# Kernel tuning notes

Hardware: AMD Instinct MI355X
Metric: run time of the kernel (lower is better)

The kernel has to match this reference:

```python
import jax, jax.numpy as jnp
import numpy as np

A, B, N, D, E = 2, 128, 50000, 512, 4096  # atomics, batch, entities, feat dim, nnz per sparse row-matrix
CLIP = 1e-14


def setup_inputs() -> dict:
    key = jax.random.key(0)
    ks = jax.random.split(key, 7)
    return {
        "entity_embedding": jax.random.normal(ks[0], (N, D), jnp.float32) * 0.02,
        "head_vector": jax.random.uniform(ks[1], (A, B, N), jnp.float32),
        "head_emb": jax.random.normal(ks[2], (A, B, D), jnp.float32),
        "pred_emb": jax.random.normal(ks[3], (A, B, D), jnp.float32),
        "edge_val": jax.random.uniform(ks[4], (A, B, E), jnp.float32),
        "edge_src": jax.random.randint(ks[5], (A, B, E), 0, N),
        "edge_dst": jax.random.randint(ks[6], (A, B, E), 0, N),
    }


def clip_norm(v):
    # masked_fill(v < clip, 0) / max(clip, sum(v, -1))
    v = jnp.where(v < CLIP, 0.0, v)
    return v / jnp.maximum(CLIP, jnp.sum(v, axis=-1, keepdims=True))


def reference(entity_embedding, head_vector, head_emb, pred_emb, edge_val, edge_src, edge_dst):
    a, b, n = head_vector.shape
    # --- symbolic message passing: per-(atomic, batch) sparse spmv via gather/scatter ---
    # msg over edge e: val[e] * head_vector[src[e]], scattered into dst[e]
    msgs = edge_val * jnp.take_along_axis(head_vector, edge_src, axis=-1)  # [A,B,E]
    offs = (jnp.arange(a * b, dtype=edge_dst.dtype) * n).reshape(a, b, 1)
    flat_idx = (edge_dst + offs).reshape(-1)
    symbolic = (
        jnp.zeros((a * b * n,), head_vector.dtype)
        .at[flat_idx].add(msgs.reshape(-1))
        .reshape(a, b, n)
    )
    symbolic = clip_norm(symbolic)
    # --- neural enhancement: estimate tail emb (TransE-style), softmax KGE scores over all entities ---
    tail_emb = head_emb + pred_emb                                  # estimate_tail_emb
    score = jnp.einsum('abd,nd->abn', tail_emb, entity_embedding)   # kge_similarity
    neural = jax.nn.softmax(score, axis=-1)                         # [A,B,N]
    enhanced = clip_norm(symbolic + neural)
    # --- product conjunction over atomics targeting the same free term ---
    agg = clip_norm(jnp.prod(enhanced, axis=0))                     # [B,N]
    # --- fuzzy_vector_to_embedding ---
    out_emb = agg @ entity_embedding                                # [B,D]
    return out_emb
```

## Files before the change

kernel.cpp:

```cpp
#include <hip/hip_runtime.h>
#include <hip/hip_bf16.h>
#include <cstdint>
#include <cstddef>

#define A_ 2
#define B_ 128
#define N_ 50000
#define D_ 512
#define E_ 4096
#define AB_ 256
#define CLIPV 1e-14f

static const size_t OFF_SYM   = 0;
static const size_t OFF_SCORE = 12800000;
static const size_t OFF_AGG   = 19200000;
static const size_t OFF_TAIL  = 25600000;
static const size_t OFF_STATS = 25731072;
#define ST_SYMSUM 0
#define ST_EXPSUM 512
#define ST_AGGSUM 1024
#define CH_K 768
#define OCHUNK 66
#define PSTRIDE 800
#define SBLKS 782

typedef __attribute__((ext_vector_type(8))) short short8;
typedef __attribute__((ext_vector_type(4))) float f32x4;

__device__ __forceinline__ unsigned short to_bf16(float f) {
    __hip_bfloat16 bh = __float2bfloat16(f);
    return *reinterpret_cast<unsigned short*>(&bh);
}
__device__ __forceinline__ float bf16f(unsigned short b) {
    return __uint_as_float(((unsigned int)b) << 16);
}
__device__ __forceinline__ void gld_lds16(const unsigned short* g, unsigned short* l) {
    __builtin_amdgcn_global_load_lds(
        (const __attribute__((address_space(1))) void*)g,
        (__attribute__((address_space(3))) void*)l, 16, 0, 0);
}
__device__ __forceinline__ short8 cvt8(const float4& a, const float4& b) {
    short8 h;
    h[0]=(short)to_bf16(a.x); h[1]=(short)to_bf16(a.y); h[2]=(short)to_bf16(a.z); h[3]=(short)to_bf16(a.w);
    h[4]=(short)to_bf16(b.x); h[5]=(short)to_bf16(b.y); h[6]=(short)to_bf16(b.z); h[7]=(short)to_bf16(b.w);
    return h;
}

__global__ __launch_bounds__(256) void k_tail(const float* __restrict__ head,
                                              const float* __restrict__ pred,
                                              unsigned short* __restrict__ tail_hi) {
    int i = blockIdx.x * 256 + threadIdx.x;
    if (i < AB_ * D_) {
        float t = head[i] + pred[i];
        tail_hi[i] = to_bf16(t);
    }
}

__global__ __launch_bounds__(256) void k_scatter(const float* __restrict__ hv,
                                                 const float* __restrict__ ev,
                                                 const int* __restrict__ es,
                                                 const int* __restrict__ ed,
                                                 float* __restrict__ sym,
                                                 float* __restrict__ stats) {
    int ab = blockIdx.x;
    float* symr = sym + (size_t)ab * N_;
    float4 z = make_float4(0.f, 0.f, 0.f, 0.f);
    float4* symv = reinterpret_cast<float4*>(symr);
    for (int i = threadIdx.x; i < 12500; i += 256) symv[i] = z;
    __syncthreads();
    const float* hvr = hv + (size_t)ab * N_;
    int base = ab * E_;
    float local = 0.f;
    for (int e = threadIdx.x; e < E_; e += 256) {
        float v = ev[base + e];
        int s = es[base + e];
        int d = ed[base + e];
        float m = v * hvr[s];
        local += m;
        atomicAdd(&symr[d], m);
    }
    __shared__ float red[256];
    red[threadIdx.x] = local;
    __syncthreads();
    for (int st = 128; st > 0; st >>= 1) {
        if (threadIdx.x < st) red[threadIdx.x] += red[threadIdx.x + st];
        __syncthreads();
    }
    if (threadIdx.x == 0) stats[ST_SYMSUM + ab] = red[0];
}

#define SCB_OFF 8192
#define SBPITCH 32

__global__ __launch_bounds__(256) void k_score(const float* __restrict__ ent,
                                               const unsigned short* __restrict__ tail_hi,
                                               unsigned short* __restrict__ p_out,
                                               float* __restrict__ parts) {
    __shared__ unsigned short lds[12288];
    const int tid = threadIdx.x;
    const int w = tid >> 6;
    const int l = tid & 63;
    const int lm = l & 15;
    const int kg = l >> 4;
    const int n0 = blockIdx.x * 64;
    const int m0w = w * 64;

    f32x4 acc[4][4];
    #pragma unroll
    for (int i = 0; i < 4; ++i)
        #pragma unroll
        for (int j = 0; j < 4; ++j) acc[i][j] = (f32x4){0.f, 0.f, 0.f, 0.f};

    const int arow_base = w * 16 + (l >> 2);
    const int ak = (l & 3) * 8;
    const int bn = tid >> 2;
    const int bc = tid & 3;
    int entrow = n0 + bn;
    if (entrow > N_ - 1) entrow = N_ - 1;
    const float* entp = ent + (size_t)entrow * D_ + bc * 8;

    float4 rB0 = *reinterpret_cast<const float4*>(entp);
    float4 rB1 = *reinterpret_cast<const float4*>(entp + 4);

    for (int t = 0; t < 16; ++t) {
        const int k0 = t * 32;
        #pragma unroll
        for (int i = 0; i < 4; ++i) {
            int row = arow_base + i * 64;
            gld_lds16(tail_hi + (size_t)row * D_ + k0 + ak, &lds[w * 512 + i * 2048]);
        }
        *reinterpret_cast<short8*>(&lds[SCB_OFF + bn * SBPITCH + bc * 8]) = cvt8(rB0, rB1);
        __syncthreads();
        if (t < 15) {
            const int k1 = k0 + 32;
            rB0 = *reinterpret_cast<const float4*>(entp + k1);
            rB1 = *reinterpret_cast<const float4*>(entp + k1 + 4);
        }
        short8 bh[4];
        #pragma unroll
        for (int nj = 0; nj < 4; ++nj) {
            int br = nj * 16 + lm;
            bh[nj] = *reinterpret_cast<const short8*>(&lds[SCB_OFF + br * SBPITCH + kg * 8]);
        }
        #pragma unroll
        for (int mi = 0; mi < 4; ++mi) {
            int ar = m0w + mi * 16 + lm;
            short8 ah = *reinterpret_cast<const short8*>(&lds[ar * 32 + kg * 8]);
            #pragma unroll
            for (int nj = 0; nj < 4; ++nj)
                acc[mi][nj] = __builtin_amdgcn_mfma_f32_16x16x32_bf16(ah, bh[nj], acc[mi][nj], 0, 0, 0);
        }
        if (t < 15) __syncthreads();
    }

    #pragma unroll
    for (int mi = 0; mi < 4; ++mi) {
        #pragma unroll
        for (int j = 0; j < 4; ++j) {
            int row = m0w + mi * 16 + kg * 4 + j;
            float rsum = 0.f;
            #pragma unroll
            for (int nj = 0; nj < 4; ++nj) {
                int col = n0 + nj * 16 + lm;
                if (col < N_) {
                    float pv = expf(acc[mi][nj][j]);
                    p_out[(size_t)row * N_ + col] = to_bf16(pv);
                    rsum += pv;
                }
            }
            rsum += __shfl_xor(rsum, 1);
            rsum += __shfl_xor(rsum, 2);
            rsum += __shfl_xor(rsum, 4);
            rsum += __shfl_xor(rsum, 8);
            if (lm == 0) parts[(size_t)row * PSTRIDE + blockIdx.x] = rsum;
        }
    }
}

__global__ __launch_bounds__(256) void k_expred(const float* __restrict__ parts,
                                                float* __restrict__ stats) {
    int row = blockIdx.x;
    float s = 0.f;
    for (int c = threadIdx.x; c < SBLKS; c += 256) s += parts[(size_t)row * PSTRIDE + c];
    __shared__ float red[256];
    red[threadIdx.x] = s;
    __syncthreads();
    for (int st = 128; st > 0; st >>= 1) {
        if (threadIdx.x < st) red[threadIdx.x] += red[threadIdx.x + st];
        __syncthreads();
    }
    if (threadIdx.x == 0) stats[ST_EXPSUM + row] = red[0];
}

__global__ __launch_bounds__(256) void k_enhagg(const unsigned short* __restrict__ p,
                                                const float* __restrict__ sym,
                                                float* __restrict__ agg,
                                                float* __restrict__ stats) {
    int b = blockIdx.x >> 2, part = blockIdx.x & 3;
    size_t off0 = (size_t)b * N_ + part * 12500;
    size_t off1 = (size_t)(128 + b) * N_ + part * 12500;
    float is0 = 1.f / fmaxf(CLIPV, stats[ST_SYMSUM + b]);
    float is1 = 1.f / fmaxf(CLIPV, stats[ST_SYMSUM + 128 + b]);
    float ie0 = 1.f / fmaxf(CLIPV, stats[ST_EXPSUM + b]);
    float ie1 = 1.f / fmaxf(CLIPV, stats[ST_EXPSUM + 128 + b]);
    const float4* s0p = reinterpret_cast<const float4*>(sym + off0);
    const float4* s1p = reinterpret_cast<const float4*>(sym + off1);
    const ushort4* p0p = reinterpret_cast<const ushort4*>(p + off0);
    const ushort4* p1p = reinterpret_cast<const ushort4*>(p + off1);
    float4* aggp = reinterpret_cast<float4*>(agg + off0);
    float local = 0.f;
    for (int i = threadIdx.x; i < 3125; i += 256) {
        float4 s0 = s0p[i], s1 = s1p[i];
        ushort4 q0 = p0p[i], q1 = p1p[i];
        float sv0[4] = {s0.x, s0.y, s0.z, s0.w};
        float sv1[4] = {s1.x, s1.y, s1.z, s1.w};
        float qv0[4] = {bf16f(q0.x), bf16f(q0.y), bf16f(q0.z), bf16f(q0.w)};
        float qv1[4] = {bf16f(q1.x), bf16f(q1.y), bf16f(q1.z), bf16f(q1.w)};
        float vv[4];
        #pragma unroll
        for (int c = 0; c < 4; ++c) {
            float a0 = (sv0[c] < CLIPV) ? 0.f : sv0[c];
            float a1 = (sv1[c] < CLIPV) ? 0.f : sv1[c];
            float e0 = a0 * is0 + qv0[c] * ie0; e0 = (e0 < CLIPV) ? 0.f : e0;
            float e1 = a1 * is1 + qv1[c] * ie1; e1 = (e1 < CLIPV) ? 0.f : e1;
            float v = e0 * e1 * 0.25f;
            v = (v < CLIPV) ? 0.f : v;
            local += v;
            vv[c] = v;
        }
        float4 o; o.x = vv[0]; o.y = vv[1]; o.z = vv[2]; o.w = vv[3];
        aggp[i] = o;
    }
    __shared__ float red[256];
    red[threadIdx.x] = local;
    __syncthreads();
    for (int st = 128; st > 0; st >>= 1) {
        if (threadIdx.x < st) red[threadIdx.x] += red[threadIdx.x + st];
        __syncthreads();
    }
    if (threadIdx.x == 0) atomicAdd(&stats[ST_AGGSUM + b], red[0]);
}

#define APITCH 40
#define OG_BUF 10240
#define OLDS_B 5120

__global__ __launch_bounds__(256) void k_outgemm(const float* __restrict__ ent,
                                                 const float* __restrict__ aggf,
                                                 float* __restrict__ part) {
    __shared__ unsigned short lds[20480];
    const int bid = blockIdx.x;
    const int chunk = bid >> 2, dt = bid & 3;
    const int n0 = chunk * CH_K, d0 = dt * 128;
    const int tid = threadIdx.x;
    const int w = tid >> 6;
    const int l = tid & 63;
    const int lm = l & 15;
    const int kg = l >> 4;
    const int m0w = (w >> 1) * 64;
    const int c0w = (w & 1) * 64;

    f32x4 acc[4][4];
    #pragma unroll
    for (int i = 0; i < 4; ++i)
        #pragma unroll
        for (int j = 0; j < 4; ++j) acc[i][j] = (f32x4){0.f, 0.f, 0.f, 0.f};

    const int arow = tid >> 1;
    const int ahalf = tid & 1;
    const int dcol = tid & 127;
    const int bhalf = tid >> 7;
    const size_t entcol = (size_t)(d0 + dcol);

    float ra[16], rb[16];

    auto loadA = [&](int k0) {
        int nbase = n0 + k0 + ahalf * 16;
        const float* asrc = aggf + (size_t)arow * N_ + nbase;
        #pragma unroll
        for (int c = 0; c < 2; ++c) {
            if (nbase + c * 8 + 7 < N_) {
                float4 g0 = *reinterpret_cast<const float4*>(asrc + c * 8);
                float4 g1 = *reinterpret_cast<const float4*>(asrc + c * 8 + 4);
                ra[c*8+0]=g0.x; ra[c*8+1]=g0.y; ra[c*8+2]=g0.z; ra[c*8+3]=g0.w;
                ra[c*8+4]=g1.x; ra[c*8+5]=g1.y; ra[c*8+6]=g1.z; ra[c*8+7]=g1.w;
            } else {
                #pragma unroll
                for (int j = 0; j < 8; ++j) {
                    int n = nbase + c * 8 + j;
                    ra[c*8+j] = (n < N_) ? aggf[(size_t)arow * N_ + n] : 0.f;
                }
            }
        }
    };
    auto loadB = [&](int k0) {
        int nb = n0 + k0 + bhalf * 16;
        #pragma unroll
        for (int j = 0; j < 16; ++j) {
            int n = nb + j;
            if (n > N_ - 1) n = N_ - 1;
            rb[j] = ent[(size_t)n * D_ + entcol];
        }
    };
    auto stage = [&](int bufbase) {
        #pragma unroll
        for (int c = 0; c < 2; ++c) {
            short8 hb;
            #pragma unroll
            for (int j = 0; j < 8; ++j) hb[j] = (short)to_bf16(ra[c*8+j]);
            *reinterpret_cast<short8*>(&lds[bufbase + arow * APITCH + ahalf * 16 + c * 8]) = hb;
        }
        #pragma unroll
        for (int c = 0; c < 2; ++c) {
            short8 hb;
            #pragma unroll
            for (int j = 0; j < 8; ++j) hb[j] = (short)to_bf16(rb[c*8+j]);
            *reinterpret_cast<short8*>(&lds[bufbase + OLDS_B + dcol * APITCH + bhalf * 16 + c * 8]) = hb;
        }
    };

    loadA(0); loadB(0);
    stage(0);
    loadA(32); loadB(32);
    __syncthreads();

    for (int t = 0; t < 24; ++t) {
        const int base = (t & 1) * OG_BUF;
        const int nb2 = ((t + 1) & 1) * OG_BUF;
        if (t < 23) stage(nb2);
        if (t < 22) { loadA((t + 2) * 32); loadB((t + 2) * 32); }
        short8 ah[4], bh[4];
        #pragma unroll
        for (int mi = 0; mi < 4; ++mi) {
            int r = m0w + mi * 16 + lm;
            ah[mi] = *reinterpret_cast<const short8*>(&lds[base + r * APITCH + kg * 8]);
        }
        #pragma unroll
        for (int nj = 0; nj < 4; ++nj) {
            int r = c0w + nj * 16 + lm;
            bh[nj] = *reinterpret_cast<const short8*>(&lds[base + OLDS_B + r * APITCH + kg * 8]);
        }
        #pragma unroll
        for (int mi = 0; mi < 4; ++mi)
            #pragma unroll
            for (int nj = 0; nj < 4; ++nj)
                acc[mi][nj] = __builtin_amdgcn_mfma_f32_16x16x32_bf16(ah[mi], bh[nj], acc[mi][nj], 0, 0, 0);
        __syncthreads();
    }

    float* pbase = part + (size_t)chunk * 65536;
    #pragma unroll
    for (int nj = 0; nj < 4; ++nj) {
        int dcolo = d0 + c0w + nj * 16 + lm;
        #pragma unroll
        for (int mi = 0; mi < 4; ++mi) {
            int brow = m0w + mi * 16 + kg * 4;
            #pragma unroll
            for (int j = 0; j < 4; ++j)
                pbase[(size_t)(brow + j) * 512 + dcolo] = acc[mi][nj][j];
        }
    }
}

__global__ __launch_bounds__(256) void k_redout(const float* __restrict__ part,
                                                const float* __restrict__ stats,
                                                float* __restrict__ out) {
    int i = blockIdx.x * 256 + threadIdx.x;
    int b = i >> 9;
    float s = 0.f;
    for (int c = 0; c < OCHUNK; ++c) s += part[(size_t)c * 65536 + i];
    out[i] = s / fmaxf(CLIPV, stats[ST_AGGSUM + b]);
}

extern "C" void kernel_launch(void* const* d_in, const int* in_sizes, int n_in,
                              void* d_out, int out_size, void* d_ws, size_t ws_size,
                              hipStream_t stream) {
    const float* ent = (const float*)d_in[0];
    const float* hv  = (const float*)d_in[1];
    const float* he  = (const float*)d_in[2];
    const float* pe  = (const float*)d_in[3];
    const float* ev  = (const float*)d_in[4];
    const int*   es  = (const int*)d_in[5];
    const int*   ed  = (const int*)d_in[6];
    float* out = (float*)d_out;
    float* ws = (float*)d_ws;

    unsigned short* tail_hi = (unsigned short*)(ws + OFF_TAIL);
    unsigned short* p_bf16 = (unsigned short*)(ws + OFF_SCORE);
    float* parts = ws + OFF_AGG;
    float* aggf  = ws + OFF_AGG;
    float* stats = ws + OFF_STATS;

    hipMemsetAsync(stats, 0, 2048 * sizeof(float), stream);

    k_tail<<<512, 256, 0, stream>>>(he, pe, tail_hi);
    k_scatter<<<AB_, 256, 0, stream>>>(hv, ev, es, ed, ws + OFF_SYM, stats);
    k_score<<<SBLKS, 256, 0, stream>>>(ent, tail_hi, p_bf16, parts);
    k_expred<<<AB_, 256, 0, stream>>>(parts, stats);
    k_enhagg<<<B_ * 4, 256, 0, stream>>>(p_bf16, ws + OFF_SYM, aggf, stats);
    k_outgemm<<<OCHUNK * 4, 256, 0, stream>>>(ent, aggf, ws + OFF_SYM);
    k_redout<<<256, 256, 0, stream>>>(ws + OFF_SYM, stats, out);
}
```

Before: 194.7 us.

## Double K-step to 64 and XOR-swizzle LDS tiles in score GEMM

The score GEMM kernel now loads a 64-wide K slice per iteration instead of 32, which halves the loop trips and the barriers. A and B tiles in LDS use a 64-element row pitch with an XOR swizzle on 8-element chunks to avoid bank conflicts on the MFMA operand reads. LDS use per block grows from about 24KB to 40KB, and more B registers are prefetched, which may lower occupancy.

```diff
diff --git a/kernel.cpp b/kernel.cpp
--- a/kernel.cpp
+++ b/kernel.cpp
@@ -89,14 +89,13 @@
     if (threadIdx.x == 0) stats[ST_SYMSUM + ab] = red[0];
 }
 
-#define SCB_OFF 8192
-#define SBPITCH 32
+#define SCB_OFF 16384
 
 __global__ __launch_bounds__(256) void k_score(const float* __restrict__ ent,
                                                const unsigned short* __restrict__ tail_hi,
                                                unsigned short* __restrict__ p_out,
                                                float* __restrict__ parts) {
-    __shared__ unsigned short lds[12288];
+    __shared__ unsigned short lds[20480];
     const int tid = threadIdx.x;
     const int w = tid >> 6;
     const int l = tid & 63;
@@ -111,46 +110,58 @@
         #pragma unroll
         for (int j = 0; j < 4; ++j) acc[i][j] = (f32x4){0.f, 0.f, 0.f, 0.f};
 
-    const int arow_base = w * 16 + (l >> 2);
-    const int ak = (l & 3) * 8;
+    const int arow_off = l >> 3;
+    const int asrc_kc = ((l & 7) ^ (l >> 3)) * 8;
     const int bn = tid >> 2;
-    const int bc = tid & 3;
+    const int bs = tid & 3;
     int entrow = n0 + bn;
     if (entrow > N_ - 1) entrow = N_ - 1;
-    const float* entp = ent + (size_t)entrow * D_ + bc * 8;
+    const float* entp = ent + (size_t)entrow * D_ + bs * 16;
+    const int bw0 = ((2 * bs)     ^ (bn & 7)) * 8;
+    const int bw1 = ((2 * bs + 1) ^ (bn & 7)) * 8;
 
     float4 rB0 = *reinterpret_cast<const float4*>(entp);
     float4 rB1 = *reinterpret_cast<const float4*>(entp + 4);
-
-    for (int t = 0; t < 16; ++t) {
-        const int k0 = t * 32;
-        #pragma unroll
-        for (int i = 0; i < 4; ++i) {
-            int row = arow_base + i * 64;
-            gld_lds16(tail_hi + (size_t)row * D_ + k0 + ak, &lds[w * 512 + i * 2048]);
-        }
-        *reinterpret_cast<short8*>(&lds[SCB_OFF + bn * SBPITCH + bc * 8]) = cvt8(rB0, rB1);
+    float4 rB2 = *reinterpret_cast<const float4*>(entp + 8);
+    float4 rB3 = *reinterpret_cast<const float4*>(entp + 12);
+
+    for (int t = 0; t < 8; ++t) {
+        const int k0 = t * 64;
+        #pragma unroll
+        for (int i = 0; i < 8; ++i) {
+            int g = w * 8 + i;
+            int row = g * 8 + arow_off;
+            gld_lds16(tail_hi + (size_t)row * D_ + k0 + asrc_kc, &lds[g * 512 + (l & 63) * 8 - (l & 63) * 8 + l * 8]);
+        }
+        *reinterpret_cast<short8*>(&lds[SCB_OFF + bn * 64 + bw0]) = cvt8(rB0, rB1);
+        *reinterpret_cast<short8*>(&lds[SCB_OFF + bn * 64 + bw1]) = cvt8(rB2, rB3);
         __syncthreads();
-        if (t < 15) {
-            const int k1 = k0 + 32;
+        if (t < 7) {
+            const int k1 = k0 + 64;
             rB0 = *reinterpret_cast<const float4*>(entp + k1);
             rB1 = *reinterpret_cast<const float4*>(entp + k1 + 4);
-        }
-        short8 bh[4];
-        #pragma unroll
-        for (int nj = 0; nj < 4; ++nj) {
-            int br = nj * 16 + lm;
-            bh[nj] = *reinterpret_cast<const short8*>(&lds[SCB_OFF + br * SBPITCH + kg * 8]);
-        }
-        #pragma unroll
-        for (int mi = 0; mi < 4; ++mi) {
-            int ar = m0w + mi * 16 + lm;
-            short8 ah = *reinterpret_cast<const short8*>(&lds[ar * 32 + kg * 8]);
-            #pragma unroll
-            for (int nj = 0; nj < 4; ++nj)
-                acc[mi][nj] = __builtin_amdgcn_mfma_f32_16x16x32_bf16(ah, bh[nj], acc[mi][nj], 0, 0, 0);
-        }
-        if (t < 15) __syncthreads();
+            rB2 = *reinterpret_cast<const float4*>(entp + k1 + 8);
+            rB3 = *reinterpret_cast<const float4*>(entp + k1 + 12);
+        }
+        #pragma unroll
+        for (int ks = 0; ks < 2; ++ks) {
+            const int c = ks * 4 + kg;
+            short8 bh[4];
+            #pragma unroll
+            for (int nj = 0; nj < 4; ++nj) {
+                int br = nj * 16 + lm;
+                bh[nj] = *reinterpret_cast<const short8*>(&lds[SCB_OFF + br * 64 + (c ^ (br & 7)) * 8]);
+            }
+            #pragma unroll
+            for (int mi = 0; mi < 4; ++mi) {
+                int ar = m0w + mi * 16 + lm;
+                short8 ah = *reinterpret_cast<const short8*>(&lds[ar * 64 + (c ^ (ar & 7)) * 8]);
+                #pragma unroll
+                for (int nj = 0; nj < 4; ++nj)
+                    acc[mi][nj] = __builtin_amdgcn_mfma_f32_16x16x32_bf16(ah, bh[nj], acc[mi][nj], 0, 0, 0);
+            }
+        }
+        if (t < 7) __syncthreads();
     }
 
     #pragma unroll
```

After: 197.9 us. No clear change (+1.6%).
